# Kernel tuning notes

Hardware: AMD Instinct MI355X
Metric: run time of the kernel (lower is better)

Reference implementation:

```python
import jax, jax.numpy as jnp
import numpy as np

N_NODES = 50000
N_EDGES = 800000
D_IN = 128
D_OUT = 128


def setup_inputs() -> dict:
    key = jax.random.key(0)
    k1, k2, k3, k4, k5, k6 = jax.random.split(key, 6)
    stdv = 1.0 / np.sqrt(D_OUT)
    x = jax.random.normal(k1, (N_NODES, D_IN), dtype=jnp.float32)
    weight = jax.random.uniform(k2, (D_IN, D_OUT), dtype=jnp.float32, minval=-stdv, maxval=stdv)
    bias = jax.random.uniform(k3, (D_OUT,), dtype=jnp.float32, minval=-stdv, maxval=stdv)
    edge_weight = jax.random.uniform(k4, (N_EDGES,), dtype=jnp.float32)
    edge_row = jax.random.randint(k5, (N_EDGES,), 0, N_NODES, dtype=jnp.int64)
    edge_col = jax.random.randint(k6, (N_EDGES,), 0, N_NODES, dtype=jnp.int64)
    return {"x": x, "weight": weight, "bias": bias,
            "edge_weight": edge_weight, "edge_row": edge_row, "edge_col": edge_col}


def reference(x, weight, bias, edge_weight, edge_row, edge_col):
    # support = input @ W   -> [N, D_OUT]
    support = x @ weight
    # spmm(adj, support): out[i] = sum over edges (i<-j) of a_ij * support[j]
    gathered = support[edge_col] * edge_weight[:, None]  # [E, D_OUT]
    out = jax.ops.segment_sum(gathered, edge_row, num_segments=N_NODES)
    return out + bias
```

## Files before the change

### kernel.cpp

```cpp
#include <hip/hip_runtime.h>
#include <hip/hip_bf16.h>

#define NN 50000
#define NE 800000
#define D 128

#define RPB 128
#define NB 391
#define NBP 1024
#define CAP 2560
#define TILE 4096
#define NBIN 196
#define TSTR 136

#define CASTB 1563
#define PACKB 4

#define XH_OFF   0
#define WF_OFF   3200000
#define CUR_OFF  3208192
#define REC_OFF  3209216

typedef short bf16x8 __attribute__((ext_vector_type(8)));
typedef float f32x4 __attribute__((ext_vector_type(4)));

__device__ inline unsigned short f2bf_u(float f) {
    __hip_bfloat16 h = __float2bfloat16(f);
    return __builtin_bit_cast(unsigned short, h);
}
__device__ inline unsigned pack2(float a, float b) {
    return (unsigned)f2bf_u(a) | ((unsigned)f2bf_u(b) << 16);
}
__device__ inline void acc8(float* acc, uint4 v, float w) {
    unsigned dw[4] = {v.x, v.y, v.z, v.w};
    #pragma unroll
    for (int i = 0; i < 4; ++i) {
        float lo = __int_as_float((int)(dw[i] << 16));
        float hi = __int_as_float((int)(dw[i] & 0xffff0000u));
        acc[2 * i]     += w * lo;
        acc[2 * i + 1] += w * hi;
    }
}

__global__ __launch_bounds__(512) void cast_bin_kernel(
    const float* __restrict__ x, const float* __restrict__ W,
    const int* __restrict__ erow, const int* __restrict__ ecol,
    const float* __restrict__ ew,
    unsigned* __restrict__ x_h4, unsigned short* __restrict__ Wf,
    int* __restrict__ cursor, int2* __restrict__ recs)
{
    __shared__ int  lhist[NBP];
    __shared__ int  lexcl[NBP];
    __shared__ int  lbase[NBP];
    __shared__ int  lpair[512];
    __shared__ int2 stag[TILE];

    int b = blockIdx.x;
    int t = threadIdx.x;

    if (b < CASTB) {
        int idx = b * 512 + t;
        if (idx < 800000) {
            const float4* x4 = (const float4*)x;
            float4 v0 = x4[idx * 2];
            float4 v1 = x4[idx * 2 + 1];
            uint4 o;
            o.x = pack2(v0.x, v0.y);
            o.y = pack2(v0.z, v0.w);
            o.z = pack2(v1.x, v1.y);
            o.w = pack2(v1.z, v1.w);
            ((uint4*)x_h4)[idx] = o;
        }
        return;
    }
    if (b < CASTB + PACKB) {
        int flat = (b - CASTB) * 512 + t;
        int lane = flat & 63;
        int c    = (flat >> 6) & 3;
        int nt   = flat >> 8;
        int col  = nt * 16 + (lane & 15);
        int kb   = c * 32 + (lane >> 4) * 8;
        unsigned d[4];
        #pragma unroll
        for (int jj = 0; jj < 4; ++jj) {
            float a  = W[(kb + 2 * jj) * D + col];
            float bb = W[(kb + 2 * jj + 1) * D + col];
            d[jj] = pack2(a, bb);
        }
        uint4 o; o.x = d[0]; o.y = d[1]; o.z = d[2]; o.w = d[3];
        ((uint4*)Wf)[flat] = o;
        return;
    }

    int base = (b - CASTB - PACKB) * TILE;
    int cnt = NE - base; if (cnt > TILE) cnt = TILE;

    lhist[t] = 0;
    lhist[t + 512] = 0;
    __syncthreads();

    int4 r[2], c[2]; float4 w[2]; bool val[2];
    #pragma unroll
    for (int g = 0; g < 2; ++g) {
        int i4 = (base >> 2) + t + g * 512;
        val[g] = (i4 * 4) < NE;
        if (val[g]) {
            r[g] = ((const int4*)erow)[i4];
            c[g] = ((const int4*)ecol)[i4];
            w[g] = ((const float4*)ew)[i4];
        }
    }
    #pragma unroll
    for (int g = 0; g < 2; ++g) {
        if (val[g]) {
            atomicAdd(&lhist[(unsigned)r[g].x >> 7], 1);
            atomicAdd(&lhist[(unsigned)r[g].y >> 7], 1);
            atomicAdd(&lhist[(unsigned)r[g].z >> 7], 1);
            atomicAdd(&lhist[(unsigned)r[g].w >> 7], 1);
        }
    }
    __syncthreads();

    int a0 = lhist[2 * t], a1 = lhist[2 * t + 1];
    lpair[t] = a0 + a1;
    __syncthreads();
    for (int off = 1; off < 512; off <<= 1) {
        int v = (t >= off) ? lpair[t - off] : 0;
        __syncthreads();
        lpair[t] += v;
        __syncthreads();
    }
    int exclp = lpair[t] - (a0 + a1);
    lexcl[2 * t]     = exclp;
    lexcl[2 * t + 1] = exclp + a0;
    lbase[2 * t]     = a0 ? atomicAdd(&cursor[2 * t], a0) : 0;
    lbase[2 * t + 1] = a1 ? atomicAdd(&cursor[2 * t + 1], a1) : 0;
    lhist[2 * t]     = exclp;
    lhist[2 * t + 1] = exclp + a0;
    __syncthreads();

    #pragma unroll
    for (int g = 0; g < 2; ++g) {
        if (val[g]) {
            int rr[4] = {r[g].x, r[g].y, r[g].z, r[g].w};
            int cc[4] = {c[g].x, c[g].y, c[g].z, c[g].w};
            float wwv[4] = {w[g].x, w[g].y, w[g].z, w[g].w};
            #pragma unroll
            for (int j = 0; j < 4; ++j) {
                int bk = (unsigned)rr[j] >> 7;
                int rank = atomicAdd(&lhist[bk], 1);
                int2 rec;
                rec.x = (rr[j] << 16) | cc[j];
                rec.y = __float_as_int(wwv[j]);
                stag[rank] = rec;
            }
        }
    }
    __syncthreads();

    #pragma unroll
    for (int k = 0; k < 8; ++k) {
        int i = t + k * 512;
        if (i < cnt) {
            int2 rec = stag[i];
            int bk = (((unsigned)rec.x) >> 16) >> 7;
            int pos = lbase[bk] + (i - lexcl[bk]);
            if (pos < CAP)
                recs[(size_t)bk * CAP + pos] = rec;
        }
    }
}

__global__ __launch_bounds__(512, 4) void gat_gemm_kernel(
    const unsigned short* __restrict__ x_h, const int2* __restrict__ recs,
    const int* __restrict__ cursor, const unsigned short* __restrict__ Wf,
    const float* __restrict__ bias, float* __restrict__ out)
{
    __shared__ int2 srec[CAP];
    __shared__ __align__(16) unsigned short tile[RPB * TSTR];
    __shared__ int rowstart[RPB + 1];
    __shared__ int rowcur[RPB];
    __shared__ int wtot;

    int t = threadIdx.x;
    int b = blockIdx.x;
    int cnt = cursor[b];
    if (cnt > CAP) cnt = CAP;
    const int2* my = recs + (size_t)b * CAP;
    int rb = b * RPB;

    if (t < RPB) rowcur[t] = 0;
    __syncthreads();

    int2 rr[5];
    bool vv[5];
    #pragma unroll
    for (int k = 0; k < 5; ++k) {
        int i = t + k * 512;
        vv[k] = i < cnt;
        if (vv[k]) rr[k] = my[i];
    }
    #pragma unroll
    for (int k = 0; k < 5; ++k)
        if (vv[k]) atomicAdd(&rowcur[(((unsigned)rr[k].x) >> 16) & (RPB - 1)], 1);
    __syncthreads();

    if (t < RPB) {
        int myc = rowcur[t];
        int s = myc;
        #pragma unroll
        for (int off = 1; off < 64; off <<= 1) {
            int v = __shfl_up(s, off);
            if ((t & 63) >= off) s += v;
        }
        if (t == 63) wtot = s;
        __syncthreads();
        if (t >= 64) s += wtot;
        rowstart[t] = s - myc;
        rowcur[t]   = s - myc;
    } else {
        __syncthreads();
    }
    if (t == 0) rowstart[RPB] = cnt;
    __syncthreads();

    #pragma unroll
    for (int k = 0; k < 5; ++k)
        if (vv[k]) srec[atomicAdd(&rowcur[(((unsigned)rr[k].x) >> 16) & (RPB - 1)], 1)] = rr[k];
    __syncthreads();

    int q = t & 15;
    int grp = t >> 4;
    const uint4* xv = (const uint4*)x_h;
    #pragma unroll
    for (int it = 0; it < 4; ++it) {
        int rl = it * 32 + grp;
        int p = rowstart[rl], p1 = rowstart[rl + 1];
        float acc[8] = {};
        for (; p + 8 <= p1; p += 8) {
            int2 e0 = srec[p];
            int2 e1 = srec[p + 1];
            int2 e2 = srec[p + 2];
            int2 e3 = srec[p + 3];
            int2 e4 = srec[p + 4];
            int2 e5 = srec[p + 5];
            int2 e6 = srec[p + 6];
            int2 e7 = srec[p + 7];
            uint4 w0 = xv[(size_t)(e0.x & 0xffff) * 16 + q];
            uint4 w1 = xv[(size_t)(e1.x & 0xffff) * 16 + q];
            uint4 w2 = xv[(size_t)(e2.x & 0xffff) * 16 + q];
            uint4 w3 = xv[(size_t)(e3.x & 0xffff) * 16 + q];
            uint4 w4 = xv[(size_t)(e4.x & 0xffff) * 16 + q];
            uint4 w5 = xv[(size_t)(e5.x & 0xffff) * 16 + q];
            uint4 w6 = xv[(size_t)(e6.x & 0xffff) * 16 + q];
            uint4 w7 = xv[(size_t)(e7.x & 0xffff) * 16 + q];
            acc8(acc, w0, __int_as_float(e0.y));
            acc8(acc, w1, __int_as_float(e1.y));
            acc8(acc, w2, __int_as_float(e2.y));
            acc8(acc, w3, __int_as_float(e3.y));
            acc8(acc, w4, __int_as_float(e4.y));
            acc8(acc, w5, __int_as_float(e5.y));
            acc8(acc, w6, __int_as_float(e6.y));
            acc8(acc, w7, __int_as_float(e7.y));
        }
        for (; p + 4 <= p1; p += 4) {
            int2 e0 = srec[p];
            int2 e1 = srec[p + 1];
            int2 e2 = srec[p + 2];
            int2 e3 = srec[p + 3];
            uint4 w0 = xv[(size_t)(e0.x & 0xffff) * 16 + q];
            uint4 w1 = xv[(size_t)(e1.x & 0xffff) * 16 + q];
            uint4 w2 = xv[(size_t)(e2.x & 0xffff) * 16 + q];
            uint4 w3 = xv[(size_t)(e3.x & 0xffff) * 16 + q];
            acc8(acc, w0, __int_as_float(e0.y));
            acc8(acc, w1, __int_as_float(e1.y));
            acc8(acc, w2, __int_as_float(e2.y));
            acc8(acc, w3, __int_as_float(e3.y));
        }
        for (; p < p1; ++p) {
            int2 e = srec[p];
            uint4 w = xv[(size_t)(e.x & 0xffff) * 16 + q];
            acc8(acc, w, __int_as_float(e.y));
        }
        uint4 o;
        o.x = pack2(acc[0], acc[1]);
        o.y = pack2(acc[2], acc[3]);
        o.z = pack2(acc[4], acc[5]);
        o.w = pack2(acc[6], acc[7]);
        *(uint4*)&tile[rl * TSTR + q * 8] = o;
    }
    __syncthreads();

    int wave = t >> 6, lane = t & 63;
    int m = lane & 15, quad = lane >> 4;
    const bf16x8* bp = (const bf16x8*)Wf;
    bf16x8 bfr[4];
    #pragma unroll
    for (int c = 0; c < 4; ++c) bfr[c] = bp[(wave * 4 + c) * 64 + lane];
    float bcol = bias[wave * 16 + m];

    #pragma unroll
    for (int mt = 0; mt < 8; ++mt) {
        f32x4 acc = {0.f, 0.f, 0.f, 0.f};
        #pragma unroll
        for (int c = 0; c < 4; ++c) {
            bf16x8 afr = *(const bf16x8*)&tile[(mt * 16 + m) * TSTR + c * 32 + quad * 8];
            acc = __builtin_amdgcn_mfma_f32_16x16x32_bf16(afr, bfr[c], acc, 0, 0, 0);
        }
        #pragma unroll
        for (int r = 0; r < 4; ++r) {
            int lr = mt * 16 + quad * 4 + r;
            int grow = rb + lr;
            if (grow < NN)
                out[(size_t)grow * D + wave * 16 + m] = acc[r] + bcol;
        }
    }
}

extern "C" void kernel_launch(void* const* d_in, const int* in_sizes, int n_in,
                              void* d_out, int out_size, void* d_ws, size_t ws_size,
                              hipStream_t stream) {
    const float* x    = (const float*)d_in[0];
    const float* W    = (const float*)d_in[1];
    const float* bias = (const float*)d_in[2];
    const float* ew   = (const float*)d_in[3];
    const int*   erow = (const int*)d_in[4];
    const int*   ecol = (const int*)d_in[5];
    float* out = (float*)d_out;

    unsigned* ws_u = (unsigned*)d_ws;
    unsigned*        x_h4   = ws_u + XH_OFF;
    unsigned short*  x_h    = (unsigned short*)x_h4;
    unsigned short*  Wf     = (unsigned short*)(ws_u + WF_OFF);
    int*             cursor = (int*)(ws_u + CUR_OFF);
    int2*            recs   = (int2*)(ws_u + REC_OFF);

    hipMemsetAsync(cursor, 0, NBP * sizeof(int), stream);
    cast_bin_kernel<<<CASTB + PACKB + NBIN, 512, 0, stream>>>(
        x, W, erow, ecol, ew, x_h4, Wf, cursor, recs);
    gat_gemm_kernel<<<NB, 512, 0, stream>>>(x_h, recs, cursor, Wf, bias, out);
}
```

Before: 134.2 us.

## Simplify edge binning to direct scatter and schedule binning blocks first

```diff
diff --git a/kernel.cpp b/kernel.cpp
--- a/kernel.cpp
+++ b/kernel.cpp
@@ -7,11 +7,11 @@
 
 #define RPB 128
 #define NB 391
-#define NBP 1024
 #define CAP 2560
-#define TILE 4096
-#define NBIN 196
+#define TILE 8192
+#define NBIN 98
 #define TSTR 136
+#define CURN 512
 
 #define CASTB 1563
 #define PACKB 4
@@ -49,32 +49,68 @@
     unsigned* __restrict__ x_h4, unsigned short* __restrict__ Wf,
     int* __restrict__ cursor, int2* __restrict__ recs)
 {
-    __shared__ int  lhist[NBP];
-    __shared__ int  lexcl[NBP];
-    __shared__ int  lbase[NBP];
-    __shared__ int  lpair[512];
-    __shared__ int2 stag[TILE];
+    __shared__ int lhist[CURN];
 
     int b = blockIdx.x;
     int t = threadIdx.x;
 
-    if (b < CASTB) {
-        int idx = b * 512 + t;
-        if (idx < 800000) {
-            const float4* x4 = (const float4*)x;
-            float4 v0 = x4[idx * 2];
-            float4 v1 = x4[idx * 2 + 1];
-            uint4 o;
-            o.x = pack2(v0.x, v0.y);
-            o.y = pack2(v0.z, v0.w);
-            o.z = pack2(v1.x, v1.y);
-            o.w = pack2(v1.z, v1.w);
-            ((uint4*)x_h4)[idx] = o;
+    if (b < NBIN) {
+        lhist[t] = 0;
+        __syncthreads();
+
+        int base = b * TILE;
+        int4 r[4], c[4]; float4 w[4]; bool val[4];
+        #pragma unroll
+        for (int g = 0; g < 4; ++g) {
+            int i4 = (base >> 2) + t + g * 512;
+            val[g] = (i4 * 4) < NE;
+            if (val[g]) {
+                r[g] = ((const int4*)erow)[i4];
+                c[g] = ((const int4*)ecol)[i4];
+                w[g] = ((const float4*)ew)[i4];
+            }
+        }
+        #pragma unroll
+        for (int g = 0; g < 4; ++g) {
+            if (val[g]) {
+                atomicAdd(&lhist[(unsigned)r[g].x >> 7], 1);
+                atomicAdd(&lhist[(unsigned)r[g].y >> 7], 1);
+                atomicAdd(&lhist[(unsigned)r[g].z >> 7], 1);
+                atomicAdd(&lhist[(unsigned)r[g].w >> 7], 1);
+            }
+        }
+        __syncthreads();
+
+        {
+            int n = lhist[t];
+            if (n > 0) lhist[t] = atomicAdd(&cursor[t], n);
+        }
+        __syncthreads();
+
+        #pragma unroll
+        for (int g = 0; g < 4; ++g) {
+            if (val[g]) {
+                int rr[4] = {r[g].x, r[g].y, r[g].z, r[g].w};
+                int cc[4] = {c[g].x, c[g].y, c[g].z, c[g].w};
+                float wwv[4] = {w[g].x, w[g].y, w[g].z, w[g].w};
+                #pragma unroll
+                for (int j = 0; j < 4; ++j) {
+                    int bk = (unsigned)rr[j] >> 7;
+                    int pos = atomicAdd(&lhist[bk], 1);
+                    if (pos < CAP) {
+                        int2 rec;
+                        rec.x = (rr[j] << 16) | cc[j];
+                        rec.y = __float_as_int(wwv[j]);
+                        recs[(size_t)bk * CAP + pos] = rec;
+                    }
+                }
+            }
         }
         return;
     }
-    if (b < CASTB + PACKB) {
-        int flat = (b - CASTB) * 512 + t;
+
+    if (b < NBIN + PACKB) {
+        int flat = (b - NBIN) * 512 + t;
         int lane = flat & 63;
         int c    = (flat >> 6) & 3;
         int nt   = flat >> 8;
@@ -92,82 +128,17 @@
         return;
     }
 
-    int base = (b - CASTB - PACKB) * TILE;
-    int cnt = NE - base; if (cnt > TILE) cnt = TILE;
-
-    lhist[t] = 0;
-    lhist[t + 512] = 0;
-    __syncthreads();
-
-    int4 r[2], c[2]; float4 w[2]; bool val[2];
-    #pragma unroll
-    for (int g = 0; g < 2; ++g) {
-        int i4 = (base >> 2) + t + g * 512;
-        val[g] = (i4 * 4) < NE;
-        if (val[g]) {
-            r[g] = ((const int4*)erow)[i4];
-            c[g] = ((const int4*)ecol)[i4];
-            w[g] = ((const float4*)ew)[i4];
-        }
-    }
-    #pragma unroll
-    for (int g = 0; g < 2; ++g) {
-        if (val[g]) {
-            atomicAdd(&lhist[(unsigned)r[g].x >> 7], 1);
-            atomicAdd(&lhist[(unsigned)r[g].y >> 7], 1);
-            atomicAdd(&lhist[(unsigned)r[g].z >> 7], 1);
-            atomicAdd(&lhist[(unsigned)r[g].w >> 7], 1);
-        }
-    }
-    __syncthreads();
-
-    int a0 = lhist[2 * t], a1 = lhist[2 * t + 1];
-    lpair[t] = a0 + a1;
-    __syncthreads();
-    for (int off = 1; off < 512; off <<= 1) {
-        int v = (t >= off) ? lpair[t - off] : 0;
-        __syncthreads();
-        lpair[t] += v;
-        __syncthreads();
-    }
-    int exclp = lpair[t] - (a0 + a1);
-    lexcl[2 * t]     = exclp;
-    lexcl[2 * t + 1] = exclp + a0;
-    lbase[2 * t]     = a0 ? atomicAdd(&cursor[2 * t], a0) : 0;
-    lbase[2 * t + 1] = a1 ? atomicAdd(&cursor[2 * t + 1], a1) : 0;
-    lhist[2 * t]     = exclp;
-    lhist[2 * t + 1] = exclp + a0;
-    __syncthreads();
-
-    #pragma unroll
-    for (int g = 0; g < 2; ++g) {
-        if (val[g]) {
-            int rr[4] = {r[g].x, r[g].y, r[g].z, r[g].w};
-            int cc[4] = {c[g].x, c[g].y, c[g].z, c[g].w};
-            float wwv[4] = {w[g].x, w[g].y, w[g].z, w[g].w};
-            #pragma unroll
-            for (int j = 0; j < 4; ++j) {
-                int bk = (unsigned)rr[j] >> 7;
-                int rank = atomicAdd(&lhist[bk], 1);
-                int2 rec;
-                rec.x = (rr[j] << 16) | cc[j];
-                rec.y = __float_as_int(wwv[j]);
-                stag[rank] = rec;
-            }
-        }
-    }
-    __syncthreads();
-
-    #pragma unroll
-    for (int k = 0; k < 8; ++k) {
-        int i = t + k * 512;
-        if (i < cnt) {
-            int2 rec = stag[i];
-            int bk = (((unsigned)rec.x) >> 16) >> 7;
-            int pos = lbase[bk] + (i - lexcl[bk]);
-            if (pos < CAP)
-                recs[(size_t)bk * CAP + pos] = rec;
-        }
+    int idx = (b - NBIN - PACKB) * 512 + t;
+    if (idx < 800000) {
+        const float4* x4 = (const float4*)x;
+        float4 v0 = x4[idx * 2];
+        float4 v1 = x4[idx * 2 + 1];
+        uint4 o;
+        o.x = pack2(v0.x, v0.y);
+        o.y = pack2(v0.z, v0.w);
+        o.z = pack2(v1.x, v1.y);
+        o.w = pack2(v1.z, v1.w);
+        ((uint4*)x_h4)[idx] = o;
     }
 }
 
@@ -335,8 +306,8 @@
     int*             cursor = (int*)(ws_u + CUR_OFF);
     int2*            recs   = (int2*)(ws_u + REC_OFF);
 
-    hipMemsetAsync(cursor, 0, NBP * sizeof(int), stream);
-    cast_bin_kernel<<<CASTB + PACKB + NBIN, 512, 0, stream>>>(
+    hipMemsetAsync(cursor, 0, CURN * sizeof(int), stream);
+    cast_bin_kernel<<<NBIN + PACKB + CASTB, 512, 0, stream>>>(
         x, W, erow, ecol, ew, x_h4, Wf, cursor, recs);
     gat_gemm_kernel<<<NB, 512, 0, stream>>>(x_h, recs, cursor, Wf, bias, out);
 }
```

Result: faster. 130.6 us (-2.7%).
